# Performance work log

Hardware: AMD Instinct MI355X
Metric: run time of the kernel (lower is better)

The kernel has to match this reference:

```python
import jax, jax.numpy as jnp
import numpy as np


def setup_inputs() -> dict:
    key = jax.random.key(0)
    ks = jax.random.split(key, 14)
    B, T, S = 32, 64, 64
    L, H, D, V = 2, 512, 512, 32000
    s = 0.05  # weight scale to keep tanh/sigmoid unsaturated
    tokens = jax.random.randint(ks[0], (B, T), 0, V)
    embedding = jax.random.normal(ks[1], (V, D)) * s
    embedding = embedding.at[0].set(0.0)  # padding_idx=0
    inp = {
        "tokens": tokens,
        "h0": jax.random.normal(ks[2], (L, B, H)) * s,
        "c0": jax.random.normal(ks[3], (L, B, H)) * s,
        "context": jax.random.normal(ks[4], (B, S, H)),
        "embedding": embedding,
        "Wih": jax.random.normal(ks[5], (L, 4 * H, D)) * s,
        "Whh": jax.random.normal(ks[6], (L, 4 * H, H)) * s,
        "bih": jax.random.normal(ks[7], (L, 4 * H)) * s,
        "bhh": jax.random.normal(ks[8], (L, 4 * H)) * s,
        "W_attn_in": jax.random.normal(ks[9], (H, H)) * s,
        "W_attn_out": jax.random.normal(ks[10], (H, 2 * H)) * s,
        "W_lin": jax.random.normal(ks[11], (V, H)) * s,
        "b_lin": jax.random.normal(ks[12], (V,)) * s,
    }
    return inp


def reference(tokens, h0, c0, context, embedding, Wih, Whh, bih, bhh,
              W_attn_in, W_attn_out, W_lin, b_lin):
    """Per-timestep multi-layer LSTM decode + global (Luong) attention +
    linear/log-softmax. Dropout layers are identity (eval / p=0).
    tokens: [B,T] int; h0,c0: [L,B,H]; context: [B,S,H].
    Returns (log_probs [T,B,V], h_T [L,B,H], c_T [L,B,H], attn_last [B,S]).
    """
    L = h0.shape[0]
    emb = embedding[tokens]            # [B,T,D]
    emb_t = jnp.transpose(emb, (1, 0, 2))  # [T,B,D]

    def step(carry, x_t):
        h, c = carry                   # each [L,B,H]
        inp = x_t                      # [B,D]
        hs, cs = [], []
        for l in range(L):
            gates = inp @ Wih[l].T + h[l] @ Whh[l].T + bih[l] + bhh[l]
            i, f, g, o = jnp.split(gates, 4, axis=-1)
            i, f, o = jax.nn.sigmoid(i), jax.nn.sigmoid(f), jax.nn.sigmoid(o)
            g = jnp.tanh(g)
            c_l = f * c[l] + i * g
            h_l = o * jnp.tanh(c_l)
            hs.append(h_l)
            cs.append(c_l)
            inp = h_l
        h = jnp.stack(hs)
        c = jnp.stack(cs)
        # GlobalAttention: score = context . linear_in(h_top)
        q = h[-1] @ W_attn_in.T                      # [B,H]
        scores = jnp.einsum('bsh,bh->bs', context, q)
        attn = jax.nn.softmax(scores, axis=-1)       # [B,S]
        ctx = jnp.einsum('bs,bsh->bh', attn, context)
        out = jnp.tanh(jnp.concatenate([ctx, h[-1]], axis=-1) @ W_attn_out.T)
        return (h, c), (out, attn)

    (hT, cT), (outs, attns) = jax.lax.scan(step, (h0, c0), emb_t)
    # outs: [T,B,H] -> vocab logits -> log-softmax over vocab
    log_probs = jax.nn.log_softmax(outs @ W_lin.T + b_lin, axis=-1)
    return log_probs, hT, cT, attns[-1]
```

## Files before the change

### kernel.cpp

```cpp
#include <hip/hip_runtime.h>
#include <math.h>

#define T_STEPS 64
#define BATCH   32
#define SEQ     64
#define HID     512
#define VOCAB   32000
#define ABASE   16000
#define SBASE   16512
#define NBLK    256

typedef unsigned short u16;
typedef unsigned int   u32;

typedef __attribute__((ext_vector_type(8))) short short8;
typedef __attribute__((ext_vector_type(4))) float f32x4;

#define AS_RLX __ATOMIC_RELAXED
#define SC_AGT __HIP_MEMORY_SCOPE_AGENT

__device__ __forceinline__ u16 f2bf(float f) {
  u32 x = __float_as_uint(f);
  u32 r = (x + 0x7fffu + ((x >> 16) & 1u)) >> 16;
  return (u16)r;
}
__device__ __forceinline__ float sigf(float x) { return 1.0f / (1.0f + expf(-x)); }

__device__ __forceinline__ float* stP(float* o, int i) {
  return o + (size_t)(i >> 6) * VOCAB + SBASE + (i & 63);
}

__device__ __forceinline__ void bst(float* p, float v) {
  __hip_atomic_store(p, v, AS_RLX, SC_AGT);
}
__device__ __forceinline__ float bld(const float* p) {
  return __hip_atomic_load(p, AS_RLX, SC_AGT);
}
__device__ __forceinline__ float4 bld4(const float* p) {
  float4 r;
  r.x = __hip_atomic_load(p + 0, AS_RLX, SC_AGT);
  r.y = __hip_atomic_load(p + 1, AS_RLX, SC_AGT);
  r.z = __hip_atomic_load(p + 2, AS_RLX, SC_AGT);
  r.w = __hip_atomic_load(p + 3, AS_RLX, SC_AGT);
  return r;
}

__device__ __forceinline__ unsigned* syncW(float* o, int i) {
  return (unsigned*)(o + (size_t)(i >> 6) * VOCAB + 17024 + (i & 63));
}

__device__ __forceinline__ void spin_until(unsigned* w, unsigned g) {
  int k = 0;
  while (__hip_atomic_load(w, AS_RLX, SC_AGT) < g) {
    __builtin_amdgcn_s_sleep(2);
    if (++k == 16384) { k = 0; __threadfence(); }
  }
}

__device__ __forceinline__ void gsync(float* o, unsigned g) {
  asm volatile("s_waitcnt vmcnt(0)" ::: "memory");
  __syncthreads();
  const int tid = threadIdx.x;
  if (blockIdx.x == 0) {
    if (tid >= 1) spin_until(syncW(o, tid), g);
    __syncthreads();
    if (tid == 0)
      __hip_atomic_store(syncW(o, 320), g, AS_RLX, SC_AGT);
  } else {
    if (tid == 0) {
      __hip_atomic_store(syncW(o, blockIdx.x), g, AS_RLX, SC_AGT);
      spin_until(syncW(o, 320), g);
    }
  }
  __syncthreads();
}

__device__ __forceinline__ int xslot(int k4, int bb) {
  return (k4 * 32 + (bb ^ (k4 & 7))) * 4;
}
__device__ __forceinline__ void stage_band(float* o, int base, float* xs) {
  const int tid = threadIdx.x;
#pragma unroll
  for (int it = 0; it < 16; ++it) {
    int f = it * 256 + tid;
    int bb = f >> 7, k4 = f & 127;
    *(float4*)&xs[xslot(k4, bb)] = bld4(stP(o, base + bb * 512 + k4 * 4));
  }
}
__device__ __forceinline__ void stage_emb(const int* __restrict__ tokens,
                                          const float* __restrict__ emb,
                                          int t, float* xs) {
  const int tid = threadIdx.x;
#pragma unroll
  for (int it = 0; it < 16; ++it) {
    int f = it * 256 + tid;
    int bb = f >> 7, k4 = f & 127;
    int tok = tokens[bb * T_STEPS + t];
    *(float4*)&xs[xslot(k4, bb)] = *(const float4*)(emb + (size_t)tok * HID + k4 * 4);
  }
}
template <int N>
__device__ __forceinline__ float dotN(const float* xs, const float* wrow,
                                      int k4base, int wofs, int bb) {
  float ax = 0.f, ay = 0.f, az = 0.f, aw = 0.f;
#pragma unroll 8
  for (int i = 0; i < N; ++i) {
    int k4 = k4base + i;
    float4 x = *(const float4*)&xs[xslot(k4, bb)];
    float4 w = *(const float4*)&wrow[wofs + i * 4];
    ax += w.x * x.x; ay += w.y * x.y; az += w.z * x.z; aw += w.w * x.w;
  }
  return (ax + ay) + (az + aw);
}
__device__ __forceinline__ void gate_tail(float* o, const float* glx, float* cs,
                                          int bk, int hout_base, int tl) {
  int b2 = tl & 31, du = tl >> 5, u = bk * 2 + du;
  float iv = sigf(glx[du * 32 + b2]);
  float fv = sigf(glx[(2 + du) * 32 + b2]);
  float gv = tanhf(glx[(4 + du) * 32 + b2]);
  float ov = sigf(glx[(6 + du) * 32 + b2]);
  float cn = fv * cs[du * 32 + b2] + iv * gv;
  cs[du * 32 + b2] = cn;
  bst(stP(o, hout_base + b2 * 512 + u), ov * tanhf(cn));
}

#define SMEM_FLOATS 37336
#define SMEM_BYTES  (SMEM_FLOATS * 4)

__global__ void __launch_bounds__(256, 1) persist_kernel(
    float* o, const int* __restrict__ tokens, const float* __restrict__ emb,
    const float* __restrict__ Wih, const float* __restrict__ Whh,
    const float* __restrict__ bih, const float* __restrict__ bhh,
    const float* __restrict__ Wai, const float* __restrict__ Wao,
    const float* __restrict__ h0in, const float* __restrict__ c0in,
    const float* __restrict__ context,
    float* __restrict__ o_h, float* __restrict__ o_c, float* __restrict__ o_attn)
{
  extern __shared__ float smem[];
  float* wih0  = smem;
  float* whh0  = smem + 4096;
  float* wih1  = smem + 8192;
  float* whh1  = smem + 12288;
  float* waiL  = smem + 16384;
  float* waoL  = smem + 17408;
  float* xs    = smem + 19456;
  float* gl    = smem + 35840;
  float* gl2   = smem + 36096;
  float* gl3   = smem + 36352;
  float* glo   = smem + 36608;
  float* oph   = smem + 36864;
  float* c0s   = smem + 37120;
  float* c1s   = smem + 37184;
  float* bias0 = smem + 37248;
  float* bias1 = smem + 37256;
  float* at_s  = smem + 37264;

  const int tid = threadIdx.x;
  const int bk  = blockIdx.x;
  const int b   = tid & 31;
  const int gq  = tid >> 5;
  unsigned g = 0;

  for (int f = tid; f < 1024; f += 256) {
    int r = f >> 7, k4 = f & 127;
    size_t j0 = (size_t)((r >> 1) * HID + bk * 2 + (r & 1));
    *(float4*)&wih0[r * 512 + k4 * 4] = *(const float4*)(Wih + j0 * HID + k4 * 4);
    *(float4*)&whh0[r * 512 + k4 * 4] = *(const float4*)(Whh + j0 * HID + k4 * 4);
    *(float4*)&wih1[r * 512 + k4 * 4] = *(const float4*)(Wih + 1048576 + j0 * HID + k4 * 4);
    *(float4*)&whh1[r * 512 + k4 * 4] = *(const float4*)(Whh + 1048576 + j0 * HID + k4 * 4);
  }
  {
    int r = tid >> 7, k4 = tid & 127;
    *(float4*)&waiL[r * 512 + k4 * 4] =
        *(const float4*)(Wai + (size_t)(bk * 2 + r) * HID + k4 * 4);
  }
  for (int f = tid; f < 512; f += 256) {
    int r = f >> 8, k4 = f & 255;
    *(float4*)&waoL[r * 1024 + k4 * 4] =
        *(const float4*)(Wao + (size_t)(bk * 2 + r) * 2 * HID + k4 * 4);
  }
  if (tid < 8) {
    int j0 = (tid >> 1) * HID + bk * 2 + (tid & 1);
    bias0[tid] = bih[j0] + bhh[j0];
    bias1[tid] = bih[2048 + j0] + bhh[2048 + j0];
  }
  if (tid < 64) {
    int b2 = tid & 31, du = tid >> 5, u = bk * 2 + du;
    c0s[du * 32 + b2] = c0in[b2 * 512 + u];
    c1s[du * 32 + b2] = c0in[16384 + b2 * 512 + u];
    bst(stP(o, 16384 + b2 * 512 + u), h0in[b2 * 512 + u]);
    bst(stP(o, 49152 + b2 * 512 + u), h0in[16384 + b2 * 512 + u]);
  }
  gsync(o, ++g);

  {
    stage_emb(tokens, emb, 0, xs); __syncthreads();
    float a0 = bias0[gq] + dotN<128>(xs, &wih0[gq * 512], 0, 0, b);
    __syncthreads();
    stage_band(o, 16384, xs); __syncthreads();
    a0 += dotN<128>(xs, &whh0[gq * 512], 0, 0, b);
    gl2[tid] = a0; __syncthreads();
    if (tid >= 64 && tid < 128) gate_tail(o, gl2, c0s, bk, 0, tid - 64);
    gsync(o, ++g);
  }

  for (int t = 0; t <= T_STEPS + 2; ++t) {
    if (t >= 3) {
      stage_band(o, 98304 + ((t + 1) & 1) * 16384, xs); __syncthreads();
      float cp = 0.f;
      if (gq < 4)
        cp = dotN<64>(xs, &waoL[(gq & 1) * 1024], (gq >> 1) * 64, (gq >> 1) * 256, b);
      glo[tid] = cp; __syncthreads();
      if (tid < 64) {
        int d = tid >> 5, b2 = tid & 31;
        float* op = &oph[((t - 3) & 1) * 128];
        float s = glo[d * 32 + b2] + glo[(2 + d) * 32 + b2]
                + op[d * 32 + b2] + op[(2 + d) * 32 + b2];
        o[(size_t)((t - 3) * BATCH + b2) * VOCAB + ABASE + bk * 2 + d] = tanhf(s);
      }
      __syncthreads();
    }
    float a0 = 0.f, a1 = 0.f, qp = 0.f;
    if (t + 1 < T_STEPS) {
      stage_emb(tokens, emb, t + 1, xs); __syncthreads();
      a0 = bias0[gq] + dotN<128>(xs, &wih0[gq * 512], 0, 0, b);
      __syncthreads();
    }
    if (t < T_STEPS) {
      stage_band(o, (t & 1) * 16384, xs); __syncthreads();
      if (t + 1 < T_STEPS) a0 += dotN<128>(xs, &whh0[gq * 512], 0, 0, b);
      a1 = bias1[gq] + dotN<128>(xs, &wih1[gq * 512], 0, 0, b);
      __syncthreads();
    }
    if (t <= T_STEPS) {
      stage_band(o, 32768 + ((t + 1) & 1) * 16384, xs); __syncthreads();
      if (t < T_STEPS) a1 += dotN<128>(xs, &whh1[gq * 512], 0, 0, b);
      if (t >= 1) {
        if (gq >= 4)
          oph[((t - 1) & 1) * 128 + (gq - 4) * 32 + b] =
              dotN<64>(xs, &waoL[(gq & 1) * 1024], ((gq >> 1) - 2) * 64,
                       512 + ((gq >> 1) - 2) * 256, b);
        qp = dotN<32>(xs, &waiL[(gq & 1) * 512], (gq >> 1) * 32, (gq >> 1) * 128, b);
      }
    }
    gl[tid] = a1; gl2[tid] = a0; gl3[tid] = qp;
    __syncthreads();
    if (tid < 64) {
      if (t < T_STEPS)
        gate_tail(o, gl, c1s, bk, 32768 + (t & 1) * 16384, tid);
    } else if (tid < 128) {
      if (t + 1 < T_STEPS)
        gate_tail(o, gl2, c0s, bk, ((t + 1) & 1) * 16384, tid - 64);
    } else if (tid < 192) {
      if (t >= 1 && t <= T_STEPS) {
        int tl = tid - 128, d = tl >> 5, b2 = tl & 31;
        float s = gl3[d * 32 + b2] + gl3[(2 + d) * 32 + b2]
                + gl3[(4 + d) * 32 + b2] + gl3[(6 + d) * 32 + b2];
        bst(stP(o, 65536 + ((t - 1) & 1) * 16384 + b2 * 512 + bk * 2 + d), s);
      }
    }
    __syncthreads();
    if (t >= 2 && t <= T_STEPS + 1) {
      const int bb = bk >> 3, sl = bk & 7;
      if (tid < 128)
        *(float4*)&xs[tid * 4] =
            bld4(stP(o, 65536 + (t & 1) * 16384 + bb * 512 + tid * 4));
      __syncthreads();
      {
        int s = tid >> 2, kc = tid & 3;
        const float* crow = context + ((size_t)bb * SEQ + s) * HID + kc * 128;
        float ax = 0.f, ay = 0.f, az = 0.f, aw = 0.f;
#pragma unroll 8
        for (int i = 0; i < 32; ++i) {
          float4 c4 = *(const float4*)(crow + i * 4);
          const float* q4 = &xs[kc * 128 + i * 4];
          ax += c4.x * q4[0]; ay += c4.y * q4[1];
          az += c4.z * q4[2]; aw += c4.w * q4[3];
        }
        gl[tid] = (ax + ay) + (az + aw);
      }
      __syncthreads();
      if (tid < 64) {
        float sc = gl[tid * 4] + gl[tid * 4 + 1] + gl[tid * 4 + 2] + gl[tid * 4 + 3];
        float m = sc;
#pragma unroll
        for (int off = 32; off > 0; off >>= 1) m = fmaxf(m, __shfl_xor(m, off));
        float e = expf(sc - m);
        float su = e;
#pragma unroll
        for (int off = 32; off > 0; off >>= 1) su += __shfl_xor(su, off);
        float av = e / su;
        at_s[tid] = av;
        if (t == T_STEPS + 1 && sl == 0) o_attn[bb * SEQ + tid] = av;
      }
      __syncthreads();
      {
        int h = sl * 64 + (tid & 63), sh = tid >> 6;
        const float* cb = context + (size_t)bb * SEQ * HID + h;
        float a2 = 0.f;
#pragma unroll 8
        for (int s2 = sh * 16; s2 < sh * 16 + 16; ++s2)
          a2 += at_s[s2] * cb[(size_t)s2 * HID];
        glo[tid] = a2;
      }
      __syncthreads();
      if (tid < 64)
        bst(stP(o, 98304 + (t & 1) * 16384 + bb * 512 + sl * 64 + tid),
            glo[tid] + glo[tid + 64] + glo[tid + 128] + glo[tid + 192]);
    }
    gsync(o, ++g);
  }

  if (tid < 64) {
    int b2 = tid & 31, du = tid >> 5, u = bk * 2 + du;
    o_h[b2 * 512 + u]         = bld(stP(o, 16384 + b2 * 512 + u));
    o_h[16384 + b2 * 512 + u] = bld(stP(o, 49152 + b2 * 512 + u));
    o_c[b2 * 512 + u]         = c0s[du * 32 + b2];
    o_c[16384 + b2 * 512 + u] = c1s[du * 32 + b2];
  }
}

__device__ __forceinline__ short8 pack8(const float* p) {
  float4 a = *(const float4*)p, b = *(const float4*)(p + 4);
  short8 r;
  r[0] = (short)f2bf(a.x); r[1] = (short)f2bf(a.y);
  r[2] = (short)f2bf(a.z); r[3] = (short)f2bf(a.w);
  r[4] = (short)f2bf(b.x); r[5] = (short)f2bf(b.y);
  r[6] = (short)f2bf(b.z); r[7] = (short)f2bf(b.w);
  return r;
}

__global__ __launch_bounds__(256) void vocab_gemm_a(
    float* o, const float* __restrict__ Bw, const float* __restrict__ bias)
{
  __shared__ __align__(16) u16 As[4 * 64 * 8];
  __shared__ __align__(16) u16 Bs[4 * 64 * 8];
  const int tid = threadIdx.x;
  const int wv   = tid >> 6;
  const int lane = tid & 63;
  const int m16  = lane & 15;
  const int quad = lane >> 4;
  const int ct = (blockIdx.x < 250) ? blockIdx.x : blockIdx.x + 10;
  const int rowBase = blockIdx.y * 64;
  const int colBase = ct * 64;
  const int srow = tid >> 2;
  const int scg  = tid & 3;
  f32x4 acc[4];
#pragma unroll
  for (int nt = 0; nt < 4; ++nt)
#pragma unroll
    for (int r = 0; r < 4; ++r) acc[nt][r] = 0.f;

  for (int k0 = 0; k0 < HID; k0 += 32) {
    __syncthreads();
    *(short8*)&As[(scg * 64 + srow) * 8] =
        pack8(&o[(size_t)(rowBase + srow) * VOCAB + ABASE + k0 + scg * 8]);
    *(short8*)&Bs[(scg * 64 + srow) * 8] =
        pack8(&Bw[(size_t)(colBase + srow) * HID + k0 + scg * 8]);
    __syncthreads();
    short8 a = *(const short8*)&As[(quad * 64 + wv * 16 + m16) * 8];
#pragma unroll
    for (int nt = 0; nt < 4; ++nt) {
      short8 bfr = *(const short8*)&Bs[(quad * 64 + nt * 16 + m16) * 8];
      acc[nt] = __builtin_amdgcn_mfma_f32_16x16x32_bf16(a, bfr, acc[nt], 0, 0, 0);
    }
  }
#pragma unroll
  for (int nt = 0; nt < 4; ++nt) {
    int col = colBase + nt * 16 + m16;
    float bv = bias[col];
#pragma unroll
    for (int r = 0; r < 4; ++r) {
      int row = rowBase + wv * 16 + quad * 4 + r;
      o[(size_t)row * VOCAB + col] = acc[nt][r] + bv;
    }
  }
}

__global__ __launch_bounds__(256) void vocab_gemm_b(
    float* o, const float* __restrict__ Bw, const float* __restrict__ bias)
{
  __shared__ __align__(16) u16 As[32 * 512];
  const int tid = threadIdx.x;
  const int rowBase = blockIdx.x * 32;
  for (int i = tid; i < 2048; i += 256) {
    int r = i >> 6, kk = (i & 63) * 8;
    *(short8*)&As[r * 512 + kk] =
        pack8(&o[(size_t)(rowBase + r) * VOCAB + ABASE + kk]);
  }
  __syncthreads();
  const int lane = tid & 63, w = tid >> 6;
  const int m16 = lane & 15, quad = lane >> 4;
  const int rg = w & 1, cg = w >> 1;
  for (int ctile = 250; ctile < 260; ++ctile) {
    int colBase = ctile * 64 + cg * 32;
    f32x4 acc[2];
#pragma unroll
    for (int nt = 0; nt < 2; ++nt)
#pragma unroll
      for (int r = 0; r < 4; ++r) acc[nt][r] = 0.f;
    for (int k0 = 0; k0 < HID; k0 += 32) {
      short8 a = *(const short8*)&As[(rg * 16 + m16) * 512 + k0 + quad * 8];
#pragma unroll
      for (int nt = 0; nt < 2; ++nt) {
        short8 bfr = pack8(&Bw[(size_t)(colBase + nt * 16 + m16) * HID + k0 + quad * 8]);
        acc[nt] = __builtin_amdgcn_mfma_f32_16x16x32_bf16(a, bfr, acc[nt], 0, 0, 0);
      }
    }
#pragma unroll
    for (int nt = 0; nt < 2; ++nt) {
      int col = colBase + nt * 16 + m16;
      float bv = bias[col];
#pragma unroll
      for (int r = 0; r < 4; ++r) {
        int row = rowBase + rg * 16 + quad * 4 + r;
        o[(size_t)row * VOCAB + col] = acc[nt][r] + bv;
      }
    }
  }
}

__global__ __launch_bounds__(256) void logsoftmax_kernel(float* logits)
{
  __shared__ float red[256];
  const int tid = threadIdx.x;
  float* rowp = logits + (size_t)blockIdx.x * VOCAB;
  float mx = -1e30f;
  for (int i = tid; i < VOCAB / 4; i += 256) {
    float4 v = ((const float4*)rowp)[i];
    mx = fmaxf(mx, fmaxf(fmaxf(v.x, v.y), fmaxf(v.z, v.w)));
  }
  red[tid] = mx; __syncthreads();
  for (int s = 128; s > 0; s >>= 1) {
    if (tid < s) red[tid] = fmaxf(red[tid], red[tid + s]);
    __syncthreads();
  }
  mx = red[0]; __syncthreads();
  float sum = 0.f;
  for (int i = tid; i < VOCAB / 4; i += 256) {
    float4 v = ((const float4*)rowp)[i];
    sum += expf(v.x - mx) + expf(v.y - mx) + expf(v.z - mx) + expf(v.w - mx);
  }
  red[tid] = sum; __syncthreads();
  for (int s = 128; s > 0; s >>= 1) {
    if (tid < s) red[tid] += red[tid + s];
    __syncthreads();
  }
  float lse = mx + logf(red[0]);
  for (int i = tid; i < VOCAB / 4; i += 256) {
    float4 v = ((const float4*)rowp)[i];
    float4 ov;
    ov.x = v.x - lse; ov.y = v.y - lse; ov.z = v.z - lse; ov.w = v.w - lse;
    ((float4*)rowp)[i] = ov;
  }
}

extern "C" void kernel_launch(void* const* d_in, const int* in_sizes, int n_in,
                              void* d_out, int out_size, void* d_ws, size_t ws_size,
                              hipStream_t stream)
{
  (void)in_sizes; (void)n_in; (void)out_size; (void)d_ws; (void)ws_size;
  const int*   tokens  = (const int*)d_in[0];
  const float* h0      = (const float*)d_in[1];
  const float* c0      = (const float*)d_in[2];
  const float* context = (const float*)d_in[3];
  const float* emb     = (const float*)d_in[4];
  const float* Wih     = (const float*)d_in[5];
  const float* Whh     = (const float*)d_in[6];
  const float* bih     = (const float*)d_in[7];
  const float* bhh     = (const float*)d_in[8];
  const float* Wai     = (const float*)d_in[9];
  const float* Wao     = (const float*)d_in[10];
  const float* Wlin    = (const float*)d_in[11];
  const float* blin    = (const float*)d_in[12];

  float* o      = (float*)d_out;
  float* o_h    = o + (size_t)2048 * VOCAB;
  float* o_c    = o_h + 32768;
  float* o_attn = o_c + 32768;

  for (int r = 0; r < 6; ++r)
    hipMemsetAsync(o + (size_t)r * VOCAB + 17024, 0, 256, stream);

  hipFuncSetAttribute((const void*)persist_kernel,
                      hipFuncAttributeMaxDynamicSharedMemorySize, SMEM_BYTES);
  persist_kernel<<<NBLK, 256, SMEM_BYTES, stream>>>(
      o, tokens, emb, Wih, Whh, bih, bhh, Wai, Wao,
      h0, c0, context, o_h, o_c, o_attn);

  vocab_gemm_a<<<dim3(490, 32), 256, 0, stream>>>(o, Wlin, blin);
  vocab_gemm_b<<<64, 256, 0, stream>>>(o, Wlin, blin);
  logsoftmax_kernel<<<2048, 256, 0, stream>>>(o);
}
```

Baseline: 3.869 ms.

## Repartition per-block LSTM and attention dot products to reuse staged inputs across rows

Each thread now computes two gate rows over half the K range instead of one row over the full range. Each x load is reused for two weight rows, and whh0 and wih1 share one pass over the staged h. The attention projections (Wai, Wao) are split into 16-element K segments so all eight warps take part instead of only a subset, with partial sums reduced through shared memory during the gate/tail phase. The change cuts redundant LDS reads of the staged activations and balances work across warps in the sequential recurrent loop. In exchange it adds reduction buffers, extra shared memory and more reduction reads.

```diff
diff --git a/kernel.cpp b/kernel.cpp
--- a/kernel.cpp
+++ b/kernel.cpp
@@ -99,32 +99,74 @@
     *(float4*)&xs[xslot(k4, bb)] = *(const float4*)(emb + (size_t)tok * HID + k4 * 4);
   }
 }
-template <int N>
-__device__ __forceinline__ float dotN(const float* xs, const float* wrow,
-                                      int k4base, int wofs, int bb) {
-  float ax = 0.f, ay = 0.f, az = 0.f, aw = 0.f;
+
+__device__ __forceinline__ void dotPH(const float* xs, const float* W,
+                                      int kh, int q, int b, float& r0, float& r1) {
+  const float* w0 = W + (q * 2) * 512 + kh * 256;
+  const float* w1 = w0 + 512;
+  const int k0 = kh * 64;
+  float a0 = 0.f, a1 = 0.f, a2 = 0.f, a3 = 0.f;
 #pragma unroll 8
-  for (int i = 0; i < N; ++i) {
-    int k4 = k4base + i;
-    float4 x = *(const float4*)&xs[xslot(k4, bb)];
-    float4 w = *(const float4*)&wrow[wofs + i * 4];
-    ax += w.x * x.x; ay += w.y * x.y; az += w.z * x.z; aw += w.w * x.w;
-  }
-  return (ax + ay) + (az + aw);
-}
-__device__ __forceinline__ void gate_tail(float* o, const float* glx, float* cs,
-                                          int bk, int hout_base, int tl) {
+  for (int i = 0; i < 64; ++i) {
+    float4 x = *(const float4*)&xs[xslot(k0 + i, b)];
+    float4 u = *(const float4*)&w0[i * 4];
+    float4 v = *(const float4*)&w1[i * 4];
+    a0 += u.x * x.x + u.y * x.y; a1 += u.z * x.z + u.w * x.w;
+    a2 += v.x * x.x + v.y * x.y; a3 += v.z * x.z + v.w * x.w;
+  }
+  r0 += a0 + a1; r1 += a2 + a3;
+}
+__device__ __forceinline__ void dotPH2(const float* xs, const float* Wa, const float* Wb,
+                                       int kh, int q, int b,
+                                       float& ra0, float& ra1, float& rb0, float& rb1) {
+  const float* wa0 = Wa + (q * 2) * 512 + kh * 256; const float* wa1 = wa0 + 512;
+  const float* wb0 = Wb + (q * 2) * 512 + kh * 256; const float* wb1 = wb0 + 512;
+  const int k0 = kh * 64;
+  float p0 = 0.f, p1 = 0.f, p2 = 0.f, p3 = 0.f;
+  float s0 = 0.f, s1 = 0.f, s2 = 0.f, s3 = 0.f;
+#pragma unroll 8
+  for (int i = 0; i < 64; ++i) {
+    float4 x = *(const float4*)&xs[xslot(k0 + i, b)];
+    float4 u = *(const float4*)&wa0[i * 4];
+    float4 v = *(const float4*)&wa1[i * 4];
+    p0 += u.x * x.x + u.y * x.y; p1 += u.z * x.z + u.w * x.w;
+    p2 += v.x * x.x + v.y * x.y; p3 += v.z * x.z + v.w * x.w;
+    float4 u2 = *(const float4*)&wb0[i * 4];
+    float4 v2 = *(const float4*)&wb1[i * 4];
+    s0 += u2.x * x.x + u2.y * x.y; s1 += u2.z * x.z + u2.w * x.w;
+    s2 += v2.x * x.x + v2.y * x.y; s3 += v2.z * x.z + v2.w * x.w;
+  }
+  ra0 += p0 + p1; ra1 += p2 + p3; rb0 += s0 + s1; rb1 += s2 + s3;
+}
+__device__ __forceinline__ void dotSeg(const float* xs, const float* w0, const float* w1,
+                                       int seg, int b, float& r0, float& r1) {
+  const int k0 = seg * 16;
+  float a0 = 0.f, a1 = 0.f, a2 = 0.f, a3 = 0.f;
+#pragma unroll 8
+  for (int i = 0; i < 16; ++i) {
+    float4 x = *(const float4*)&xs[xslot(k0 + i, b)];
+    float4 u = *(const float4*)&w0[(k0 + i) * 4];
+    float4 v = *(const float4*)&w1[(k0 + i) * 4];
+    a0 += u.x * x.x + u.y * x.y; a1 += u.z * x.z + u.w * x.w;
+    a2 += v.x * x.x + v.y * x.y; a3 += v.z * x.z + v.w * x.w;
+  }
+  r0 = a0 + a1; r1 = a2 + a3;
+}
+
+__device__ __forceinline__ void gate_tail2(float* o, const float* glx, const float* bs,
+                                           float* cs, int bk, int hout_base, int tl) {
   int b2 = tl & 31, du = tl >> 5, u = bk * 2 + du;
-  float iv = sigf(glx[du * 32 + b2]);
-  float fv = sigf(glx[(2 + du) * 32 + b2]);
-  float gv = tanhf(glx[(4 + du) * 32 + b2]);
-  float ov = sigf(glx[(6 + du) * 32 + b2]);
+  float gi = glx[(0 + du) * 32 + b2] + glx[256 + (0 + du) * 32 + b2] + bs[0 + du];
+  float gf = glx[(2 + du) * 32 + b2] + glx[256 + (2 + du) * 32 + b2] + bs[2 + du];
+  float gg = glx[(4 + du) * 32 + b2] + glx[256 + (4 + du) * 32 + b2] + bs[4 + du];
+  float go = glx[(6 + du) * 32 + b2] + glx[256 + (6 + du) * 32 + b2] + bs[6 + du];
+  float iv = sigf(gi), fv = sigf(gf), gv = tanhf(gg), ov = sigf(go);
   float cn = fv * cs[du * 32 + b2] + iv * gv;
   cs[du * 32 + b2] = cn;
   bst(stP(o, hout_base + b2 * 512 + u), ov * tanhf(cn));
 }
 
-#define SMEM_FLOATS 37336
+#define SMEM_FLOATS 38864
 #define SMEM_BYTES  (SMEM_FLOATS * 4)
 
 __global__ void __launch_bounds__(256, 1) persist_kernel(
@@ -144,21 +186,23 @@
   float* waiL  = smem + 16384;
   float* waoL  = smem + 17408;
   float* xs    = smem + 19456;
-  float* gl    = smem + 35840;
-  float* gl2   = smem + 36096;
-  float* gl3   = smem + 36352;
-  float* glo   = smem + 36608;
-  float* oph   = smem + 36864;
-  float* c0s   = smem + 37120;
-  float* c1s   = smem + 37184;
-  float* bias0 = smem + 37248;
-  float* bias1 = smem + 37256;
-  float* at_s  = smem + 37264;
+  float* glL1  = smem + 35840;
+  float* glL0  = smem + 36352;
+  float* glq   = smem + 36864;
+  float* glo2  = smem + 37376;
+  float* gloC  = smem + 37888;
+  float* oph   = smem + 38400;
+  float* c0s   = smem + 38656;
+  float* c1s   = smem + 38720;
+  float* bias0 = smem + 38784;
+  float* bias1 = smem + 38792;
+  float* at_s  = smem + 38800;
 
   const int tid = threadIdx.x;
   const int bk  = blockIdx.x;
   const int b   = tid & 31;
-  const int gq  = tid >> 5;
+  const int q   = (tid >> 5) & 3;
+  const int kh  = tid >> 7;
   unsigned g = 0;
 
   for (int f = tid; f < 1024; f += 256) {
@@ -194,69 +238,91 @@
   gsync(o, ++g);
 
   {
+    float a0 = 0.f, a1 = 0.f;
     stage_emb(tokens, emb, 0, xs); __syncthreads();
-    float a0 = bias0[gq] + dotN<128>(xs, &wih0[gq * 512], 0, 0, b);
+    dotPH(xs, wih0, kh, q, b, a0, a1);
     __syncthreads();
     stage_band(o, 16384, xs); __syncthreads();
-    a0 += dotN<128>(xs, &whh0[gq * 512], 0, 0, b);
-    gl2[tid] = a0; __syncthreads();
-    if (tid >= 64 && tid < 128) gate_tail(o, gl2, c0s, bk, 0, tid - 64);
+    dotPH(xs, whh0, kh, q, b, a0, a1);
+    glL0[kh * 256 + (q * 2 + 0) * 32 + b] = a0;
+    glL0[kh * 256 + (q * 2 + 1) * 32 + b] = a1;
+    __syncthreads();
+    if (tid >= 64 && tid < 128) gate_tail2(o, glL0, bias0, c0s, bk, 0, tid - 64);
     gsync(o, ++g);
   }
 
   for (int t = 0; t <= T_STEPS + 2; ++t) {
+    const int seg = kh * 4 + q;
     if (t >= 3) {
       stage_band(o, 98304 + ((t + 1) & 1) * 16384, xs); __syncthreads();
-      float cp = 0.f;
-      if (gq < 4)
-        cp = dotN<64>(xs, &waoL[(gq & 1) * 1024], (gq >> 1) * 64, (gq >> 1) * 256, b);
-      glo[tid] = cp; __syncthreads();
+      float r0, r1;
+      dotSeg(xs, waoL, waoL + 1024, seg, b, r0, r1);
+      gloC[(0 * 8 + seg) * 32 + b] = r0;
+      gloC[(1 * 8 + seg) * 32 + b] = r1;
+      __syncthreads();
       if (tid < 64) {
-        int d = tid >> 5, b2 = tid & 31;
-        float* op = &oph[((t - 3) & 1) * 128];
-        float s = glo[d * 32 + b2] + glo[(2 + d) * 32 + b2]
-                + op[d * 32 + b2] + op[(2 + d) * 32 + b2];
-        o[(size_t)((t - 3) * BATCH + b2) * VOCAB + ABASE + bk * 2 + d] = tanhf(s);
-      }
-      __syncthreads();
-    }
-    float a0 = 0.f, a1 = 0.f, qp = 0.f;
+        int du = tid >> 5, b2 = tid & 31;
+        float s = 0.f;
+#pragma unroll
+        for (int sg = 0; sg < 8; ++sg) s += gloC[(du * 8 + sg) * 32 + b2];
+        s += oph[((t - 3) & 1) * 128 + du * 32 + b2];
+        o[(size_t)((t - 3) * BATCH + b2) * VOCAB + ABASE + bk * 2 + du] = tanhf(s);
+      }
+      __syncthreads();
+    }
+    float a0_0 = 0.f, a0_1 = 0.f, a1_0 = 0.f, a1_1 = 0.f;
     if (t + 1 < T_STEPS) {
       stage_emb(tokens, emb, t + 1, xs); __syncthreads();
-      a0 = bias0[gq] + dotN<128>(xs, &wih0[gq * 512], 0, 0, b);
+      dotPH(xs, wih0, kh, q, b, a0_0, a0_1);
       __syncthreads();
     }
     if (t < T_STEPS) {
       stage_band(o, (t & 1) * 16384, xs); __syncthreads();
-      if (t + 1 < T_STEPS) a0 += dotN<128>(xs, &whh0[gq * 512], 0, 0, b);
-      a1 = bias1[gq] + dotN<128>(xs, &wih1[gq * 512], 0, 0, b);
+      if (t + 1 < T_STEPS)
+        dotPH2(xs, whh0, wih1, kh, q, b, a0_0, a0_1, a1_0, a1_1);
+      else
+        dotPH(xs, wih1, kh, q, b, a1_0, a1_1);
       __syncthreads();
     }
     if (t <= T_STEPS) {
       stage_band(o, 32768 + ((t + 1) & 1) * 16384, xs); __syncthreads();
-      if (t < T_STEPS) a1 += dotN<128>(xs, &whh1[gq * 512], 0, 0, b);
+      if (t < T_STEPS) dotPH(xs, whh1, kh, q, b, a1_0, a1_1);
       if (t >= 1) {
-        if (gq >= 4)
-          oph[((t - 1) & 1) * 128 + (gq - 4) * 32 + b] =
-              dotN<64>(xs, &waoL[(gq & 1) * 1024], ((gq >> 1) - 2) * 64,
-                       512 + ((gq >> 1) - 2) * 256, b);
-        qp = dotN<32>(xs, &waiL[(gq & 1) * 512], (gq >> 1) * 32, (gq >> 1) * 128, b);
-      }
-    }
-    gl[tid] = a1; gl2[tid] = a0; gl3[tid] = qp;
+        float r0, r1;
+        dotSeg(xs, waiL, waiL + 512, seg, b, r0, r1);
+        glq[(0 * 8 + seg) * 32 + b] = r0;
+        glq[(1 * 8 + seg) * 32 + b] = r1;
+        dotSeg(xs, waoL + 512, waoL + 1536, seg, b, r0, r1);
+        glo2[(0 * 8 + seg) * 32 + b] = r0;
+        glo2[(1 * 8 + seg) * 32 + b] = r1;
+      }
+    }
+    glL1[kh * 256 + (q * 2 + 0) * 32 + b] = a1_0;
+    glL1[kh * 256 + (q * 2 + 1) * 32 + b] = a1_1;
+    glL0[kh * 256 + (q * 2 + 0) * 32 + b] = a0_0;
+    glL0[kh * 256 + (q * 2 + 1) * 32 + b] = a0_1;
     __syncthreads();
     if (tid < 64) {
       if (t < T_STEPS)
-        gate_tail(o, gl, c1s, bk, 32768 + (t & 1) * 16384, tid);
+        gate_tail2(o, glL1, bias1, c1s, bk, 32768 + (t & 1) * 16384, tid);
     } else if (tid < 128) {
       if (t + 1 < T_STEPS)
-        gate_tail(o, gl2, c0s, bk, ((t + 1) & 1) * 16384, tid - 64);
+        gate_tail2(o, glL0, bias0, c0s, bk, ((t + 1) & 1) * 16384, tid - 64);
     } else if (tid < 192) {
       if (t >= 1 && t <= T_STEPS) {
-        int tl = tid - 128, d = tl >> 5, b2 = tl & 31;
-        float s = gl3[d * 32 + b2] + gl3[(2 + d) * 32 + b2]
-                + gl3[(4 + d) * 32 + b2] + gl3[(6 + d) * 32 + b2];
-        bst(stP(o, 65536 + ((t - 1) & 1) * 16384 + b2 * 512 + bk * 2 + d), s);
+        int tl = tid - 128, du = tl >> 5, b2 = tl & 31;
+        float s = 0.f;
+#pragma unroll
+        for (int sg = 0; sg < 8; ++sg) s += glq[(du * 8 + sg) * 32 + b2];
+        bst(stP(o, 65536 + ((t - 1) & 1) * 16384 + b2 * 512 + bk * 2 + du), s);
+      }
+    } else {
+      if (t >= 1 && t <= T_STEPS) {
+        int tl = tid - 192, du = tl >> 5, b2 = tl & 31;
+        float s = 0.f;
+#pragma unroll
+        for (int sg = 0; sg < 8; ++sg) s += glo2[(du * 8 + sg) * 32 + b2];
+        oph[((t - 1) & 1) * 128 + du * 32 + b2] = s;
       }
     }
     __syncthreads();
@@ -277,11 +343,11 @@
           ax += c4.x * q4[0]; ay += c4.y * q4[1];
           az += c4.z * q4[2]; aw += c4.w * q4[3];
         }
-        gl[tid] = (ax + ay) + (az + aw);
+        glL1[tid] = (ax + ay) + (az + aw);
       }
       __syncthreads();
       if (tid < 64) {
-        float sc = gl[tid * 4] + gl[tid * 4 + 1] + gl[tid * 4 + 2] + gl[tid * 4 + 3];
+        float sc = glL1[tid * 4] + glL1[tid * 4 + 1] + glL1[tid * 4 + 2] + glL1[tid * 4 + 3];
         float m = sc;
 #pragma unroll
         for (int off = 32; off > 0; off >>= 1) m = fmaxf(m, __shfl_xor(m, off));
@@ -301,12 +367,12 @@
 #pragma unroll 8
         for (int s2 = sh * 16; s2 < sh * 16 + 16; ++s2)
           a2 += at_s[s2] * cb[(size_t)s2 * HID];
-        glo[tid] = a2;
+        gloC[tid] = a2;
       }
       __syncthreads();
       if (tid < 64)
         bst(stP(o, 98304 + (t & 1) * 16384 + bb * 512 + sl * 64 + tid),
-            glo[tid] + glo[tid + 64] + glo[tid + 128] + glo[tid + 192]);
+            gloC[tid] + gloC[tid + 64] + gloC[tid + 128] + gloC[tid + 192]);
     }
     gsync(o, ++g);
   }
```

New measurement: 4.023 ms. +4.0%, slower.
